# Optimization experiments

Hardware: AMD Instinct MI355X
Metric: run time of the kernel (lower is better)

The kernel has to match this reference:

```python
import jax, jax.numpy as jnp
import numpy as np

B, R, K, D = 65536, 8, 8, 256


def setup_inputs() -> dict:
    key = jax.random.key(0)
    ks = jax.random.split(key, 7)
    return {
        "fine_memory": jax.random.normal(ks[0], (B, R, D), dtype=jnp.float32),
        "compressed_memory": jax.random.normal(ks[1], (B, K, D), dtype=jnp.float32),
        "fm_count": jax.random.randint(ks[2], (B,), 0, R + 1),
        "new_segment": jax.random.normal(ks[3], (B, D), dtype=jnp.float32),
        "valid_mask": jax.random.randint(ks[4], (B,), 0, 2).astype(bool),
        "conv_w": jax.random.normal(ks[5], (D, D, 2), dtype=jnp.float32) * 0.05,
        "conv_b": jax.random.normal(ks[6], (D,), dtype=jnp.float32) * 0.05,
    }


def reference(fine_memory, compressed_memory, fm_count, new_segment, valid_mask, conv_w, conv_b):
    """Vectorized CompressiveMemory.update().

    Per sample b (only where valid_mask[b]):
      - if fm_count[b] < R: write new_segment into fm slot fm_count[b]; count += 1
      - else: c_new = Conv1d([cm_last, fm_oldest]); shift cm left, append c_new;
              shift fm left, append new_segment.
    """
    b, r, d = fine_memory.shape
    insert = valid_mask & (fm_count < r)          # (B,) append into free slot
    shift = valid_mask & (fm_count >= r)          # (B,) FIFO shift + compress

    # --- insert branch: masked one-hot scatter of new_segment at position fm_count
    onehot = (jnp.arange(r)[None, :] == fm_count[:, None]) & insert[:, None]  # (B,R)
    fm_ins = jnp.where(onehot[:, :, None], new_segment[:, None, :], fine_memory)

    # --- shift branch: compress [cm_last, fm_oldest] with 2-tap conv (out,in,k)
    c_new = (jnp.einsum('bi,oi->bo', compressed_memory[:, -1], conv_w[:, :, 0])
             + jnp.einsum('bi,oi->bo', fine_memory[:, 0], conv_w[:, :, 1])
             + conv_b)  # (B,D)
    cm_shift = jnp.concatenate([compressed_memory[:, 1:], c_new[:, None, :]], axis=1)
    fm_shift = jnp.concatenate([fine_memory[:, 1:], new_segment[:, None, :]], axis=1)

    fm_new = jnp.where(shift[:, None, None], fm_shift, fm_ins)
    cm_new = jnp.where(shift[:, None, None], cm_shift, compressed_memory)
    fm_count_new = fm_count + insert.astype(fm_count.dtype)
    return fm_new, cm_new, fm_count_new
```

## Files before the change

kernel.cpp:

```cpp
#include <hip/hip_runtime.h>


#define NB 65536
#define RR 8
#define KK 8
#define DD 256
#define WFLOATS (DD * DD * 2)
#define G 8

typedef float f4 __attribute__((ext_vector_type(4)));

static __device__ __forceinline__ f4 ntload(const float* p) {
    return __builtin_nontemporal_load((const f4*)p);
}
static __device__ __forceinline__ void ntstore(float* p, f4 v) {
    __builtin_nontemporal_store(v, (f4*)p);
}

__global__ __launch_bounds__(256) void transpose_pack(
    const float* __restrict__ W, float* __restrict__ Wt2)
{
    int t = blockIdx.x * 256 + threadIdx.x;
    int o = t >> 9;
    int m = t & 511;
    Wt2[(size_t)(m >> 2) * (DD * 4) + o * 4 + (m & 3)] = W[t];
}

static __device__ __forceinline__ void conv_inline(
    const float* __restrict__ cmb, const float* __restrict__ fmb,
    const float* __restrict__ Wt2, const float* __restrict__ bias,
    float* __restrict__ ocm, float* xbuf, int tid)
{
    xbuf[tid * 2]     = cmb[(KK - 1) * DD + tid];
    xbuf[tid * 2 + 1] = fmb[tid];
    __syncthreads();
    float acc = 0.f;
    const float* wp = Wt2 + tid * 4;
    #pragma unroll 8
    for (int m4 = 0; m4 < 128; ++m4) {
        const f4 wq = *(const f4*)(wp + (size_t)m4 * (DD * 4));
        const f4 xq = *(const f4*)&xbuf[m4 * 4];
        acc += xq.x * wq.x + xq.y * wq.y + xq.z * wq.z + xq.w * wq.w;
    }
    acc += bias[tid];
    ocm[(KK - 1) * DD + tid] = acc;
    __syncthreads();
}

__global__ __launch_bounds__(256) void fused_update(
    const float* __restrict__ fm,
    const float* __restrict__ cm,
    const int* __restrict__ cnt_in,
    const float* __restrict__ seg,
    const int* __restrict__ valid,
    const float* __restrict__ Wt2,
    const float* __restrict__ bias,
    float* __restrict__ out_fm,
    float* __restrict__ out_cm,
    float* __restrict__ out_cnt)
{
    __shared__ float xbuf[512];

    const int tid  = threadIdx.x;
    const int w    = tid >> 6;
    const int lane = tid & 63;
    const int c    = lane << 2;
    const int base = blockIdx.x * G;

    const int r0 = w, r1 = w + 4;

    int nxt_cA = cnt_in[base + 0], nxt_cB = cnt_in[base + 1];
    int nxt_vA = valid[base + 0],  nxt_vB = valid[base + 1];

    for (int j = 0; j < G; j += 2) {
        const int bA = base + j, bB = base + j + 1;
        const int cntA = nxt_cA, cntB = nxt_cB;
        const bool vA = nxt_vA != 0, vB = nxt_vB != 0;
        if (j + 2 < G) {
            nxt_cA = cnt_in[bA + 2]; nxt_cB = cnt_in[bB + 2];
            nxt_vA = valid[bA + 2];  nxt_vB = valid[bB + 2];
        }

        const bool insA = vA && (cntA < RR), shfA = vA && (cntA >= RR);
        const bool insB = vB && (cntB < RR), shfB = vB && (cntB >= RR);

        const float* fmA  = fm  + (size_t)bA * (RR * DD);
        const float* cmA  = cm  + (size_t)bA * (KK * DD);
        const float* segA = seg + (size_t)bA * DD;
        const float* fmB  = fm  + (size_t)bB * (RR * DD);
        const float* cmB  = cm  + (size_t)bB * (KK * DD);
        const float* segB = seg + (size_t)bB * DD;
        float* ofmA = out_fm + (size_t)bA * (RR * DD);
        float* ocmA = out_cm + (size_t)bA * (KK * DD);
        float* ofmB = out_fm + (size_t)bB * (RR * DD);
        float* ocmB = out_cm + (size_t)bB * (KK * DD);

        const float* f0A = shfA ? fmA + (r0 + 1) * DD
                                : (insA && r0 == cntA) ? segA : fmA + r0 * DD;
        const float* f1A = shfA ? ((r1 < 7) ? fmA + (r1 + 1) * DD : segA)
                                : (insA && r1 == cntA) ? segA : fmA + r1 * DD;
        const bool   c1A = !(shfA && r1 == 7);
        const float* c0A = cmA + (shfA ? r0 + 1 : r0) * DD;
        const float* c1Ap = c1A ? cmA + (shfA ? r1 + 1 : r1) * DD : cmA;

        const float* f0B = shfB ? fmB + (r0 + 1) * DD
                                : (insB && r0 == cntB) ? segB : fmB + r0 * DD;
        const float* f1B = shfB ? ((r1 < 7) ? fmB + (r1 + 1) * DD : segB)
                                : (insB && r1 == cntB) ? segB : fmB + r1 * DD;
        const bool   c1B = !(shfB && r1 == 7);
        const float* c0B = cmB + (shfB ? r0 + 1 : r0) * DD;
        const float* c1Bp = c1B ? cmB + (shfB ? r1 + 1 : r1) * DD : cmB;

        f4 a0 = ntload(f0A + c);
        f4 a1 = ntload(f1A + c);
        f4 a2 = ntload(c0A + c);
        f4 a3 = ntload(c1Ap + c);
        f4 b0 = ntload(f0B + c);
        f4 b1 = ntload(f1B + c);
        f4 b2 = ntload(c0B + c);
        f4 b3 = ntload(c1Bp + c);

        ntstore(ofmA + r0 * DD + c, a0);
        ntstore(ofmA + r1 * DD + c, a1);
        ntstore(ocmA + r0 * DD + c, a2);
        if (c1A) ntstore(ocmA + r1 * DD + c, a3);
        ntstore(ofmB + r0 * DD + c, b0);
        ntstore(ofmB + r1 * DD + c, b1);
        ntstore(ocmB + r0 * DD + c, b2);
        if (c1B) ntstore(ocmB + r1 * DD + c, b3);

        if (tid == 0) {
            out_cnt[bA] = (float)(cntA + (insA ? 1 : 0));
            out_cnt[bB] = (float)(cntB + (insB ? 1 : 0));
        }

        if (shfA) conv_inline(cmA, fmA, Wt2, bias, ocmA, xbuf, tid);
        if (shfB) conv_inline(cmB, fmB, Wt2, bias, ocmB, xbuf, tid);
    }
}

extern "C" void kernel_launch(void* const* d_in, const int* in_sizes, int n_in,
                              void* d_out, int out_size, void* d_ws, size_t ws_size,
                              hipStream_t stream) {
    const float* fm    = (const float*)d_in[0];
    const float* cm    = (const float*)d_in[1];
    const int*   cnt   = (const int*)d_in[2];
    const float* seg   = (const float*)d_in[3];
    const int*   valid = (const int*)d_in[4];
    const float* W     = (const float*)d_in[5];
    const float* bias  = (const float*)d_in[6];

    float* out_fm  = (float*)d_out;
    float* out_cm  = out_fm + (size_t)NB * RR * DD;
    float* out_cnt = out_cm + (size_t)NB * KK * DD;

    float* Wt2 = (float*)d_ws;

    hipLaunchKernelGGL(transpose_pack, dim3(WFLOATS / 256), dim3(256), 0, stream, W, Wt2);
    hipLaunchKernelGGL(fused_update, dim3(NB / G), dim3(256), 0, stream,
                       fm, cm, cnt, seg, valid, Wt2, bias, out_fm, out_cm, out_cnt);
}
```

Before: 446.0 us.

## Batch conv for all shifted samples in a block to reuse weight loads

Instead of running the 2-tap conv matvec separately for each shifted sample, the kernel stages the inputs of every shifted sample in the block into per-sample shared buffers. It then runs one pass over the weights that accumulates all G samples at once, so the 512 KB weight matrix is read once per block rather than once per shifted sample. The cost is more shared memory and registers, plus wasted FLOPs on slots that are not shifted, since all G accumulators are computed whenever any sample in the block shifts.

Result: no change. 448.4 us (+0.5%).

```diff
diff --git a/kernel.cpp b/kernel.cpp
--- a/kernel.cpp
+++ b/kernel.cpp
@@ -26,27 +26,6 @@
     Wt2[(size_t)(m >> 2) * (DD * 4) + o * 4 + (m & 3)] = W[t];
 }
 
-static __device__ __forceinline__ void conv_inline(
-    const float* __restrict__ cmb, const float* __restrict__ fmb,
-    const float* __restrict__ Wt2, const float* __restrict__ bias,
-    float* __restrict__ ocm, float* xbuf, int tid)
-{
-    xbuf[tid * 2]     = cmb[(KK - 1) * DD + tid];
-    xbuf[tid * 2 + 1] = fmb[tid];
-    __syncthreads();
-    float acc = 0.f;
-    const float* wp = Wt2 + tid * 4;
-    #pragma unroll 8
-    for (int m4 = 0; m4 < 128; ++m4) {
-        const f4 wq = *(const f4*)(wp + (size_t)m4 * (DD * 4));
-        const f4 xq = *(const f4*)&xbuf[m4 * 4];
-        acc += xq.x * wq.x + xq.y * wq.y + xq.z * wq.z + xq.w * wq.w;
-    }
-    acc += bias[tid];
-    ocm[(KK - 1) * DD + tid] = acc;
-    __syncthreads();
-}
-
 __global__ __launch_bounds__(256) void fused_update(
     const float* __restrict__ fm,
     const float* __restrict__ cm,
@@ -59,7 +38,7 @@
     float* __restrict__ out_cm,
     float* __restrict__ out_cnt)
 {
-    __shared__ float xbuf[512];
+    __shared__ float xbuf[G][512];
 
     const int tid  = threadIdx.x;
     const int w    = tid >> 6;
@@ -68,6 +47,7 @@
     const int base = blockIdx.x * G;
 
     const int r0 = w, r1 = w + 4;
+    int mask = 0;
 
     int nxt_cA = cnt_in[base + 0], nxt_cB = cnt_in[base + 1];
     int nxt_vA = valid[base + 0],  nxt_vB = valid[base + 1];
@@ -134,8 +114,38 @@
             out_cnt[bB] = (float)(cntB + (insB ? 1 : 0));
         }
 
-        if (shfA) conv_inline(cmA, fmA, Wt2, bias, ocmA, xbuf, tid);
-        if (shfB) conv_inline(cmB, fmB, Wt2, bias, ocmB, xbuf, tid);
+        if (shfA) {
+            xbuf[j][tid * 2]     = cmA[(KK - 1) * DD + tid];
+            xbuf[j][tid * 2 + 1] = fmA[tid];
+            mask |= 1 << j;
+        }
+        if (shfB) {
+            xbuf[j + 1][tid * 2]     = cmB[(KK - 1) * DD + tid];
+            xbuf[j + 1][tid * 2 + 1] = fmB[tid];
+            mask |= 2 << j;
+        }
+    }
+
+    if (mask) {
+        __syncthreads();
+        float acc[G];
+        #pragma unroll
+        for (int s = 0; s < G; ++s) acc[s] = 0.f;
+
+        const float* wp = Wt2 + tid * 4;
+        for (int m4 = 0; m4 < 128; ++m4) {
+            const f4 wq = *(const f4*)(wp + (size_t)m4 * (DD * 4));
+            #pragma unroll
+            for (int s = 0; s < G; ++s) {
+                const f4 xq = *(const f4*)&xbuf[s][m4 * 4];
+                acc[s] += xq.x * wq.x + xq.y * wq.y + xq.z * wq.z + xq.w * wq.w;
+            }
+        }
+        const float bv = bias[tid];
+        #pragma unroll
+        for (int s = 0; s < G; ++s)
+            if ((mask >> s) & 1)
+                out_cm[((size_t)(base + s) * KK + (KK - 1)) * DD + tid] = acc[s] + bv;
     }
 }
 
```
